# Optimization experiments

Measured on AMD Instinct MI355X. Metric: run time of the kernel, lower is better.

Reference implementation:

```python
import jax, jax.numpy as jnp
import numpy as np

B, D, H, W, C = 4, 8, 16, 16, 512
K_RED = 8
R = C // K_RED          # reduced channels for Q/K
EPS = 1e-3              # keras LayerNormalization default epsilon


def setup_inputs() -> dict:
    key = jax.random.key(0)
    ks = jax.random.split(key, 8)
    s = 0.02
    f32 = jnp.float32
    return {
        "x":  jax.random.normal(ks[0], (B, D, H, W, C), f32),
        # 1x1x1 Conv3D == per-position linear over channels
        "wq": (jax.random.normal(ks[1], (C, R), f32) * s), "bq": jnp.zeros((R,), f32),
        "wk": (jax.random.normal(ks[2], (C, R), f32) * s), "bk": jnp.zeros((R,), f32),
        "wv": (jax.random.normal(ks[3], (C, C), f32) * s), "bv": jnp.zeros((C,), f32),
        "wm": (jax.random.normal(ks[4], (C, C), f32) * s), "bm": jnp.zeros((C,), f32),
        "g1": jnp.ones((C,), f32), "b1": jnp.zeros((C,), f32),
        "g2": jnp.ones((C,), f32), "b2": jnp.zeros((C,), f32),
    }


def _layer_norm(x, g, b):
    m = jnp.mean(x, axis=-1, keepdims=True)
    v = jnp.mean(jnp.square(x - m), axis=-1, keepdims=True)
    return (x - m) * jax.lax.rsqrt(v + EPS) * g + b


def reference(x, wq, bq, wk, bk, wv, bv, wm, bm, g1, b1, g2, b2):
    b, d, h, w, c = x.shape
    f = h * w
    xf = x.reshape(b, d, f, c)                      # [B,D,F,C]
    Q = xf @ wq + bq                                # [B,D,F,R]
    K = xf @ wk + bk                                # [B,D,F,R]
    V = xf @ wv + bv                                # [B,D,F,C]
    # full global scores: [B, D, F, D, F]
    e = jnp.einsum('bifr,bgjr->bifgj', Q, K)
    alphas = jax.nn.softmax(e.reshape(b, d, f, d * f), axis=-1)
    alphas = alphas.reshape(b, d, f, d, f)
    # original einsum 'bdfgh,bdhi->bdfi' sums over key-depth g and uses V at
    # the query depth d; fold the g-sum first, then per-depth F x F matmul.
    a2 = alphas.sum(axis=3)                         # [B,D,F,F]
    attn = jnp.einsum('bdfh,bdhc->bdfc', a2, V)     # [B,D,F,C]
    y1 = _layer_norm(attn + xf, g1, b1)
    y2 = _layer_norm(y1 + jax.nn.relu(y1 @ wm + bm), g2, b2)
    return y2.reshape(b, d, h, w, c)
```

## Files before the change

kernel.cpp:

```cpp
#include <hip/hip_runtime.h>
#include <cstdint>

#define LN_EPS 1e-3f
using u16 = unsigned short;
using u32 = unsigned int;
typedef __attribute__((ext_vector_type(8))) short bh8;
typedef __attribute__((ext_vector_type(4))) float f4;
#define MFMA16(A,B,C) __builtin_amdgcn_mfma_f32_16x16x32_bf16((A),(B),(C),0,0,0)

__device__ __forceinline__ u16 bf16r(float f){
    union{float f;u32 u;} c; c.f=f;
    return (u16)((c.u + 0x7fffu + ((c.u>>16)&1u))>>16);
}
__device__ __forceinline__ u32 pk2(float a, float b){
    return (u32)bf16r(a) | ((u32)bf16r(b)<<16);
}
__device__ __forceinline__ void glds16(const void* g, void* l){
    __builtin_amdgcn_global_load_lds(
        (const __attribute__((address_space(1))) u32*)g,
        (__attribute__((address_space(3))) u32*)l, 16, 0, 0);
}

__global__ __launch_bounds__(256) void k0_prep(
    const float* __restrict__ wq, const float* __restrict__ wk,
    const float* __restrict__ wv, const float* __restrict__ wm,
    u16* __restrict__ wqkv_p, u16* __restrict__ wm_p)
{
    const int t = threadIdx.x;
    const int c = t & 15, qn = t >> 4;
    const int quad = qn & 3, ntl = qn >> 2;
    const int blk = blockIdx.x;
    if (blk < 32){
        const int s = blk >> 1, hh = blk & 1;
        const int krow = s*32 + quad*8;
        u16* dst = wqkv_p + (size_t)s*20480;
        #pragma unroll
        for (int i=0;i<5;++i){
            const int nt = hh*20 + i*4 + ntl;
            const int n = nt*16 + c;
            const float* src; int ldw;
            if (n < 64){ src = wq + (size_t)krow*64 + n; ldw = 64; }
            else if (n < 128){ src = wk + (size_t)krow*64 + (n-64); ldw = 64; }
            else { src = wv + (size_t)krow*512 + (n-128); ldw = 512; }
            float v[8];
            #pragma unroll
            for (int j=0;j<8;++j) v[j] = src[(size_t)j*ldw];
            uint4 o; o.x=pk2(v[0],v[1]); o.y=pk2(v[2],v[3]); o.z=pk2(v[4],v[5]); o.w=pk2(v[6],v[7]);
            *(uint4*)&dst[((nt*4+quad)*16 + c)*8] = o;
        }
    } else {
        const int bb = blk - 32;
        const int s = bb >> 1, hh = bb & 1;
        const int krow = s*32 + quad*8;
        u16* dst = wm_p + (size_t)s*16384;
        #pragma unroll
        for (int i=0;i<4;++i){
            const int nt = hh*16 + i*4 + ntl;
            const int n = nt*16 + c;
            const float* src = wm + (size_t)krow*512 + n;
            float v[8];
            #pragma unroll
            for (int j=0;j<8;++j) v[j] = src[(size_t)j*512];
            uint4 o; o.x=pk2(v[0],v[1]); o.y=pk2(v[2],v[3]); o.z=pk2(v[4],v[5]); o.w=pk2(v[6],v[7]);
            *(uint4*)&dst[((nt*4+quad)*16 + c)*8] = o;
        }
    }
}

__global__ __launch_bounds__(512) void k1_qkv(
    const float* __restrict__ x, const float* __restrict__ bq, const float* __restrict__ bk,
    const u16* __restrict__ wqkv_p,
    u16* __restrict__ Qb, u16* __restrict__ Kb, u16* __restrict__ Vb)
{
    __shared__ u16 Asf[16384];
    __shared__ u16 Bs[2][20480];
    const int t = threadIdx.x, w = t>>6, lane = t&63, quad = (lane>>4)&3, c = lane&15;
    const int rg = w>>2, cg = w&3;
    const int rowbase = blockIdx.x << 5;

    #pragma unroll
    for (int i=0;i<8;++i){
        const int idx = t + (i<<9);
        const int fr = idx >> 7, fc4 = idx & 127;
        float4 xv = *(const float4*)&x[(size_t)(rowbase+fr)*512 + fc4*4];
        uint2 pkv; pkv.x = pk2(xv.x,xv.y); pkv.y = pk2(xv.z,xv.w);
        const int s = fc4 >> 3, qd = (fc4 >> 1) & 3, j0 = (fc4 & 1)*4;
        *(uint2*)&Asf[(fr>>4)*8192 + s*512 + (qd*16 + (fr&15))*8 + j0] = pkv;
    }
    f4 acc[10];
    #pragma unroll
    for (int i=0;i<10;++i) acc[i] = (f4){0.f,0.f,0.f,0.f};
    #pragma unroll
    for (int i=0;i<5;++i)
        glds16((const char*)wqkv_p + (size_t)w*5120 + i*1024 + lane*16,
               (char*)Bs[0] + w*5120 + i*1024);
    __syncthreads();

    for (int s=0;s<16;++s){
        const u16* Bcur = Bs[s&1];
        if (s+1 < 16){
            #pragma unroll
            for (int i=0;i<5;++i)
                glds16((const char*)wqkv_p + (size_t)(s+1)*40960 + (size_t)w*5120 + i*1024 + lane*16,
                       (char*)Bs[(s+1)&1] + w*5120 + i*1024);
        }
        bh8 a = *(const bh8*)&Asf[rg*8192 + s*512 + (quad*16+c)*8];
        #pragma unroll
        for (int nt2=0;nt2<10;++nt2){
            bh8 bb = *(const bh8*)&Bcur[((cg*10+nt2)*4 + quad)*128 + c*8];
            acc[nt2] = MFMA16(a, bb, acc[nt2]);
        }
        __syncthreads();
    }

    const int rt = (blockIdx.x<<1) + rg;
    const int bd = rowbase >> 8;
    const int kloc = (rowbase & 255) + rg*16 + quad*4;
    const int sv = kloc >> 5, kq = (kloc >> 3) & 3, jk0 = kloc & 7;
    #pragma unroll
    for (int nt2=0;nt2<10;++nt2){
        const int colb = cg*160 + nt2*16;
        if (colb < 128){
            const bool isK = (colb >= 64);
            const int r = colb - (isK ? 64 : 0) + c;
            const float bias = isK ? bk[r] : bq[r];
            u16* dstb = (isK ? Kb : Qb) + ((size_t)(rt*2 + (r>>5))*4 + ((r>>3)&3))*128 + (r&7);
            #pragma unroll
            for (int reg=0;reg<4;++reg)
                dstb[(quad*4+reg)*8] = bf16r(acc[nt2][reg] + bias);
        } else {
            const int ntv = (colb - 128) >> 4;
            u16* dstv = Vb + (size_t)bd*131072 + (size_t)sv*16384
                           + (size_t)((ntv*4+kq)*128 + c*8 + jk0);
            ushort4 o;
            o.x = bf16r(acc[nt2][0]); o.y = bf16r(acc[nt2][1]);
            o.z = bf16r(acc[nt2][2]); o.w = bf16r(acc[nt2][3]);
            *(ushort4*)dstv = o;
        }
    }
}

__global__ __launch_bounds__(512) void k234(
    const u16* __restrict__ Qb, const u16* __restrict__ Kb, const u16* __restrict__ Vb,
    const u16* __restrict__ wm_p,
    const float* __restrict__ x, const float* __restrict__ bv,
    const float* __restrict__ g1, const float* __restrict__ b1,
    const float* __restrict__ bm, const float* __restrict__ g2, const float* __restrict__ b2,
    float* __restrict__ out)
{
    __shared__ u16 Bs[2][16384];
    __shared__ u16 y1f[16384];
    __shared__ u16 a2f[8192];
    __shared__ u16 qsf[2048];
    __shared__ float redA[2][4][16], redB[2][4][16];
    const int t = threadIdx.x, w = t>>6, lane = t&63, quad = (lane>>4)&3, c = lane&15;
    const int rg = w>>2, cg = w&3;
    const int bd = blockIdx.x & 31, ftile = blockIdx.x >> 5;
    const int b = bd >> 3;
    const int rowbase = (bd<<8) + (ftile<<5);
    const int rt00 = rowbase >> 4;
    const char* Kbase = (const char*)Kb + (size_t)b*262144;
    const char* Vbase = (const char*)Vb + (size_t)bd*262144;

    if (w < 4) glds16((const char*)Qb + (size_t)rt00*2048 + w*1024 + lane*16,
                      (char*)qsf + w*1024);
    #pragma unroll
    for (int i=0;i<2;++i)
        glds16(Kbase + (size_t)w*2048 + i*1024 + lane*16, (char*)Bs[0] + w*2048 + i*1024);
    __syncthreads();
    bh8 aq0 = *(const bh8*)&qsf[rg*1024 + (quad*16+c)*8];
    bh8 aq1 = *(const bh8*)&qsf[rg*1024 + 512 + (quad*16+c)*8];

    float lp[4] = {0.f,0.f,0.f,0.f};
    float a2r[4][2][2] = {};
    #pragma unroll
    for (int cc=0; cc<16; ++cc){
        const u16* Bcur = Bs[cc&1];
        if (cc+1 < 16){
            #pragma unroll
            for (int i=0;i<2;++i)
                glds16(Kbase + (size_t)(cc+1)*16384 + (size_t)w*2048 + i*1024 + lane*16,
                       (char*)Bs[(cc+1)&1] + w*2048 + i*1024);
        }
        f4 sa[2] = { (f4){0.f,0.f,0.f,0.f}, (f4){0.f,0.f,0.f,0.f} };
        #pragma unroll
        for (int kt=0;kt<2;++kt){
            bh8 b0 = *(const bh8*)&Bcur[(cg*2+kt)*1024 + (quad*16+c)*8];
            bh8 b1v= *(const bh8*)&Bcur[(cg*2+kt)*1024 + 512 + (quad*16+c)*8];
            sa[kt] = MFMA16(aq0, b0, sa[kt]);
            sa[kt] = MFMA16(aq1, b1v, sa[kt]);
        }
        #pragma unroll
        for (int kt=0;kt<2;++kt)
            #pragma unroll
            for (int reg=0;reg<4;++reg){
                float e = __expf(sa[kt][reg]);
                lp[reg] += e;
                a2r[reg][cc&1][kt] += e;
            }
        __syncthreads();
    }
    {
        #pragma unroll
        for (int i=0;i<4;++i)
            glds16(Vbase + (size_t)w*4096 + i*1024 + lane*16, (char*)Bs[0] + w*4096 + i*1024);
    }
    #pragma unroll
    for (int reg=0;reg<4;++reg){
        float v = lp[reg];
        v += __shfl_xor(v,1,64); v += __shfl_xor(v,2,64);
        v += __shfl_xor(v,4,64); v += __shfl_xor(v,8,64);
        lp[reg] = v;
    }
    if (c==0){
        #pragma unroll
        for (int reg=0;reg<4;++reg) redA[rg][cg][quad*4+reg] = lp[reg];
    }
    __syncthreads();
    float fac[4];
    #pragma unroll
    for (int reg=0;reg<4;++reg){
        const int q = quad*4+reg;
        fac[reg] = 1.f/(redA[rg][0][q]+redA[rg][1][q]+redA[rg][2][q]+redA[rg][3][q]);
    }
    #pragma unroll
    for (int reg=0;reg<4;++reg)
        #pragma unroll
        for (int h=0;h<2;++h)
            #pragma unroll
            for (int kt=0;kt<2;++kt){
                const int jp = h*128 + cg*32 + kt*16 + c;
                a2f[rg*4096 + (jp>>5)*512 + (((jp>>3)&3)*16 + quad*4+reg)*8 + (jp&7)]
                    = bf16r(a2r[reg][h][kt]*fac[reg]);
            }
    __syncthreads();

    f4 cacc[8];
    #pragma unroll
    for (int i=0;i<8;++i) cacc[i] = (f4){0.f,0.f,0.f,0.f};
    for (int s8=0;s8<8;++s8){
        const u16* Bcur = Bs[s8&1];
        if (s8+1 < 8){
            #pragma unroll
            for (int i=0;i<4;++i)
                glds16(Vbase + (size_t)(s8+1)*32768 + (size_t)w*4096 + i*1024 + lane*16,
                       (char*)Bs[(s8+1)&1] + w*4096 + i*1024);
        }
        bh8 a = *(const bh8*)&a2f[rg*4096 + s8*512 + (quad*16+c)*8];
        #pragma unroll
        for (int nt2=0;nt2<8;++nt2){
            bh8 bb = *(const bh8*)&Bcur[((cg*8+nt2)*4 + quad)*128 + c*8];
            cacc[nt2] = MFMA16(a, bb, cacc[nt2]);
        }
        __syncthreads();
    }

    {
        float sv4[4] = {0.f,0.f,0.f,0.f}, qv2[4] = {0.f,0.f,0.f,0.f};
        #pragma unroll
        for (int nt2=0;nt2<8;++nt2){
            const int col = cg*128 + nt2*16 + c;
            const float bvv = bv[col];
            #pragma unroll
            for (int reg=0;reg<4;++reg){
                const int row = rowbase + rg*16 + quad*4 + reg;
                float val = cacc[nt2][reg] + bvv + x[(size_t)row*512 + col];
                cacc[nt2][reg] = val;
                sv4[reg] += val; qv2[reg] = fmaf(val,val,qv2[reg]);
            }
        }
        #pragma unroll
        for (int reg=0;reg<4;++reg){
            float s1=sv4[reg], s2=qv2[reg];
            s1 += __shfl_xor(s1,1,64); s2 += __shfl_xor(s2,1,64);
            s1 += __shfl_xor(s1,2,64); s2 += __shfl_xor(s2,2,64);
            s1 += __shfl_xor(s1,4,64); s2 += __shfl_xor(s2,4,64);
            s1 += __shfl_xor(s1,8,64); s2 += __shfl_xor(s2,8,64);
            sv4[reg]=s1; qv2[reg]=s2;
        }
        if (c==0){
            #pragma unroll
            for (int reg=0;reg<4;++reg){ redA[rg][cg][quad*4+reg]=sv4[reg]; redB[rg][cg][quad*4+reg]=qv2[reg]; }
        }
        __syncthreads();
        float mean[4], rstd[4];
        #pragma unroll
        for (int reg=0;reg<4;++reg){
            const int q = quad*4+reg;
            const float S  = redA[rg][0][q]+redA[rg][1][q]+redA[rg][2][q]+redA[rg][3][q];
            const float Q2 = redB[rg][0][q]+redB[rg][1][q]+redB[rg][2][q]+redB[rg][3][q];
            const float m = S*(1.f/512.f);
            mean[reg]=m; rstd[reg]=rsqrtf(Q2*(1.f/512.f) - m*m + LN_EPS);
        }
        #pragma unroll
        for (int nt2=0;nt2<8;++nt2){
            const int col = cg*128 + nt2*16 + c;
            const float gg = g1[col], bb1 = b1[col];
            #pragma unroll
            for (int reg=0;reg<4;++reg){
                float y = (cacc[nt2][reg]-mean[reg])*rstd[reg]*gg + bb1;
                cacc[nt2][reg] = y;
                y1f[rg*8192 + (col>>5)*512 + (((col>>3)&3)*16 + quad*4+reg)*8 + (col&7)] = bf16r(y);
            }
        }
        #pragma unroll
        for (int i=0;i<4;++i)
            glds16((const char*)wm_p + (size_t)w*4096 + i*1024 + lane*16,
                   (char*)Bs[0] + w*4096 + i*1024);
        __syncthreads();
    }

    f4 dacc[8];
    #pragma unroll
    for (int i=0;i<8;++i) dacc[i] = (f4){0.f,0.f,0.f,0.f};
    for (int s=0;s<16;++s){
        const u16* Bcur = Bs[s&1];
        if (s+1 < 16){
            #pragma unroll
            for (int i=0;i<4;++i)
                glds16((const char*)wm_p + (size_t)(s+1)*32768 + (size_t)w*4096 + i*1024 + lane*16,
                       (char*)Bs[(s+1)&1] + w*4096 + i*1024);
        }
        bh8 a = *(const bh8*)&y1f[rg*8192 + s*512 + (quad*16+c)*8];
        #pragma unroll
        for (int nt2=0;nt2<8;++nt2){
            bh8 bb = *(const bh8*)&Bcur[((cg*8+nt2)*4 + quad)*128 + c*8];
            dacc[nt2] = MFMA16(a, bb, dacc[nt2]);
        }
        __syncthreads();
    }

    {
        float sv4[4] = {0.f,0.f,0.f,0.f}, qv2[4] = {0.f,0.f,0.f,0.f};
        #pragma unroll
        for (int nt2=0;nt2<8;++nt2){
            const int col = cg*128 + nt2*16 + c;
            const float bmv = bm[col];
            #pragma unroll
            for (int reg=0;reg<4;++reg){
                float hh = fmaxf(dacc[nt2][reg]+bmv, 0.f) + cacc[nt2][reg];
                dacc[nt2][reg] = hh;
                sv4[reg] += hh; qv2[reg] = fmaf(hh,hh,qv2[reg]);
            }
        }
        #pragma unroll
        for (int reg=0;reg<4;++reg){
            float s1=sv4[reg], s2=qv2[reg];
            s1 += __shfl_xor(s1,1,64); s2 += __shfl_xor(s2,1,64);
            s1 += __shfl_xor(s1,2,64); s2 += __shfl_xor(s2,2,64);
            s1 += __shfl_xor(s1,4,64); s2 += __shfl_xor(s2,4,64);
            s1 += __shfl_xor(s1,8,64); s2 += __shfl_xor(s2,8,64);
            sv4[reg]=s1; qv2[reg]=s2;
        }
        if (c==0){
            #pragma unroll
            for (int reg=0;reg<4;++reg){ redA[rg][cg][quad*4+reg]=sv4[reg]; redB[rg][cg][quad*4+reg]=qv2[reg]; }
        }
        __syncthreads();
        float mean[4], rstd[4];
        #pragma unroll
        for (int reg=0;reg<4;++reg){
            const int q = quad*4+reg;
            const float S  = redA[rg][0][q]+redA[rg][1][q]+redA[rg][2][q]+redA[rg][3][q];
            const float Q2 = redB[rg][0][q]+redB[rg][1][q]+redB[rg][2][q]+redB[rg][3][q];
            const float m = S*(1.f/512.f);
            mean[reg]=m; rstd[reg]=rsqrtf(Q2*(1.f/512.f) - m*m + LN_EPS);
        }
        #pragma unroll
        for (int nt2=0;nt2<8;++nt2){
            const int col = cg*128 + nt2*16 + c;
            const float gg = g2[col], bb2 = b2[col];
            #pragma unroll
            for (int reg=0;reg<4;++reg){
                const int row = rowbase + rg*16 + quad*4 + reg;
                out[(size_t)row*512 + col] = (dacc[nt2][reg]-mean[reg])*rstd[reg]*gg + bb2;
            }
        }
    }
}

extern "C" void kernel_launch(void* const* d_in, const int* in_sizes, int n_in,
                              void* d_out, int out_size, void* d_ws, size_t ws_size,
                              hipStream_t stream) {
    (void)in_sizes; (void)n_in; (void)out_size; (void)ws_size;
    const float* x  = (const float*)d_in[0];
    const float* wq = (const float*)d_in[1];
    const float* bq = (const float*)d_in[2];
    const float* wk = (const float*)d_in[3];
    const float* bk = (const float*)d_in[4];
    const float* wv = (const float*)d_in[5];
    const float* bv = (const float*)d_in[6];
    const float* wm = (const float*)d_in[7];
    const float* bm = (const float*)d_in[8];
    const float* g1 = (const float*)d_in[9];
    const float* b1 = (const float*)d_in[10];
    const float* g2 = (const float*)d_in[11];
    const float* b2 = (const float*)d_in[12];

    u16* wqkv_p = (u16*)d_ws;
    u16* wm_p   = wqkv_p + 327680;
    u16* Qb     = wm_p   + 262144;
    u16* Kb     = Qb     + 524288;
    u16* Vb     = Kb     + 524288;
    float* outp = (float*)d_out;

    k0_prep<<<64, 256, 0, stream>>>(wq, wk, wv, wm, wqkv_p, wm_p);
    k1_qkv <<<256, 512, 0, stream>>>(x, bq, bk, wqkv_p, Qb, Kb, Vb);
    k234   <<<256, 512, 0, stream>>>(Qb, Kb, Vb, wm_p, x, bv, g1, b1, bm, g2, b2, outp);
}
```

Before: 152.6 us.

## Use explicit vmcnt waits and raw barriers to overlap prefetch with MFMA loops

Replaces __syncthreads in the double-buffered GEMM loops with explicit s_waitcnt vmcnt(N) plus s_barrier, so the next tile's global-to-LDS loads stay in flight while the current tile is consumed. It also raises wave priority around the MFMA bursts and issues the weight prefetch in k1 before the x conversion. In the score phase, K tiles are made twice as large so there are half as many barrier steps. The hand-placed waitcnt counts must match the number of outstanding loads exactly, so a miscount would be a correctness hazard.

```diff
diff --git a/kernel.cpp b/kernel.cpp
--- a/kernel.cpp
+++ b/kernel.cpp
@@ -7,6 +7,9 @@
 typedef __attribute__((ext_vector_type(8))) short bh8;
 typedef __attribute__((ext_vector_type(4))) float f4;
 #define MFMA16(A,B,C) __builtin_amdgcn_mfma_f32_16x16x32_bf16((A),(B),(C),0,0,0)
+#define SBAR() __builtin_amdgcn_s_barrier()
+#define CFENCE() asm volatile("" ::: "memory")
+#define WAITV(N) asm volatile("s_waitcnt vmcnt(" #N ")" ::: "memory")
 
 __device__ __forceinline__ u16 bf16r(float f){
     union{float f;u32 u;} c; c.f=f;
@@ -79,6 +82,10 @@
     const int rowbase = blockIdx.x << 5;
 
     #pragma unroll
+    for (int i=0;i<5;++i)
+        glds16((const char*)wqkv_p + (size_t)w*5120 + i*1024 + lane*16,
+               (char*)Bs[0] + w*5120 + i*1024);
+    #pragma unroll
     for (int i=0;i<8;++i){
         const int idx = t + (i<<9);
         const int fr = idx >> 7, fc4 = idx & 127;
@@ -90,27 +97,29 @@
     f4 acc[10];
     #pragma unroll
     for (int i=0;i<10;++i) acc[i] = (f4){0.f,0.f,0.f,0.f};
-    #pragma unroll
-    for (int i=0;i<5;++i)
-        glds16((const char*)wqkv_p + (size_t)w*5120 + i*1024 + lane*16,
-               (char*)Bs[0] + w*5120 + i*1024);
     __syncthreads();
 
     for (int s=0;s<16;++s){
         const u16* Bcur = Bs[s&1];
+        bh8 a = *(const bh8*)&Asf[rg*8192 + s*512 + (quad*16+c)*8];
         if (s+1 < 16){
             #pragma unroll
             for (int i=0;i<5;++i)
                 glds16((const char*)wqkv_p + (size_t)(s+1)*40960 + (size_t)w*5120 + i*1024 + lane*16,
                        (char*)Bs[(s+1)&1] + w*5120 + i*1024);
-        }
-        bh8 a = *(const bh8*)&Asf[rg*8192 + s*512 + (quad*16+c)*8];
+            WAITV(5);
+        } else {
+            WAITV(0);
+        }
+        SBAR(); CFENCE();
+        __builtin_amdgcn_s_setprio(1);
         #pragma unroll
         for (int nt2=0;nt2<10;++nt2){
             bh8 bb = *(const bh8*)&Bcur[((cg*10+nt2)*4 + quad)*128 + c*8];
             acc[nt2] = MFMA16(a, bb, acc[nt2]);
         }
-        __syncthreads();
+        __builtin_amdgcn_s_setprio(0);
+        CFENCE(); SBAR();
     }
 
     const int rt = (blockIdx.x<<1) + rg;
@@ -165,46 +174,50 @@
     if (w < 4) glds16((const char*)Qb + (size_t)rt00*2048 + w*1024 + lane*16,
                       (char*)qsf + w*1024);
     #pragma unroll
-    for (int i=0;i<2;++i)
-        glds16(Kbase + (size_t)w*2048 + i*1024 + lane*16, (char*)Bs[0] + w*2048 + i*1024);
+    for (int i=0;i<4;++i)
+        glds16(Kbase + (size_t)w*4096 + i*1024 + lane*16, (char*)Bs[0] + w*4096 + i*1024);
     __syncthreads();
     bh8 aq0 = *(const bh8*)&qsf[rg*1024 + (quad*16+c)*8];
     bh8 aq1 = *(const bh8*)&qsf[rg*1024 + 512 + (quad*16+c)*8];
 
     float lp[4] = {0.f,0.f,0.f,0.f};
-    float a2r[4][2][2] = {};
-    #pragma unroll
-    for (int cc=0; cc<16; ++cc){
+    float a2r[4][4] = {};
+    for (int cc=0; cc<8; ++cc){
         const u16* Bcur = Bs[cc&1];
-        if (cc+1 < 16){
-            #pragma unroll
-            for (int i=0;i<2;++i)
-                glds16(Kbase + (size_t)(cc+1)*16384 + (size_t)w*2048 + i*1024 + lane*16,
-                       (char*)Bs[(cc+1)&1] + w*2048 + i*1024);
-        }
-        f4 sa[2] = { (f4){0.f,0.f,0.f,0.f}, (f4){0.f,0.f,0.f,0.f} };
-        #pragma unroll
-        for (int kt=0;kt<2;++kt){
-            bh8 b0 = *(const bh8*)&Bcur[(cg*2+kt)*1024 + (quad*16+c)*8];
-            bh8 b1v= *(const bh8*)&Bcur[(cg*2+kt)*1024 + 512 + (quad*16+c)*8];
+        if (cc+1 < 8){
+            #pragma unroll
+            for (int i=0;i<4;++i)
+                glds16(Kbase + (size_t)(cc+1)*32768 + (size_t)w*4096 + i*1024 + lane*16,
+                       (char*)Bs[(cc+1)&1] + w*4096 + i*1024);
+            WAITV(4);
+        } else {
+            WAITV(0);
+        }
+        SBAR(); CFENCE();
+        __builtin_amdgcn_s_setprio(1);
+        f4 sa[4];
+        #pragma unroll
+        for (int kt=0;kt<4;++kt){
+            sa[kt] = (f4){0.f,0.f,0.f,0.f};
+            bh8 b0 = *(const bh8*)&Bcur[(cg*4+kt)*1024 + (quad*16+c)*8];
+            bh8 bv1= *(const bh8*)&Bcur[(cg*4+kt)*1024 + 512 + (quad*16+c)*8];
             sa[kt] = MFMA16(aq0, b0, sa[kt]);
-            sa[kt] = MFMA16(aq1, b1v, sa[kt]);
-        }
-        #pragma unroll
-        for (int kt=0;kt<2;++kt)
+            sa[kt] = MFMA16(aq1, bv1, sa[kt]);
+        }
+        __builtin_amdgcn_s_setprio(0);
+        #pragma unroll
+        for (int kt=0;kt<4;++kt)
             #pragma unroll
             for (int reg=0;reg<4;++reg){
                 float e = __expf(sa[kt][reg]);
                 lp[reg] += e;
-                a2r[reg][cc&1][kt] += e;
+                a2r[reg][kt] += e;
             }
-        __syncthreads();
-    }
-    {
-        #pragma unroll
-        for (int i=0;i<4;++i)
-            glds16(Vbase + (size_t)w*4096 + i*1024 + lane*16, (char*)Bs[0] + w*4096 + i*1024);
-    }
+        CFENCE(); SBAR();
+    }
+    #pragma unroll
+    for (int i=0;i<4;++i)
+        glds16(Vbase + (size_t)w*4096 + i*1024 + lane*16, (char*)Bs[0] + w*4096 + i*1024);
     #pragma unroll
     for (int reg=0;reg<4;++reg){
         float v = lp[reg];
@@ -226,13 +239,11 @@
     #pragma unroll
     for (int reg=0;reg<4;++reg)
         #pragma unroll
-        for (int h=0;h<2;++h)
-            #pragma unroll
-            for (int kt=0;kt<2;++kt){
-                const int jp = h*128 + cg*32 + kt*16 + c;
-                a2f[rg*4096 + (jp>>5)*512 + (((jp>>3)&3)*16 + quad*4+reg)*8 + (jp&7)]
-                    = bf16r(a2r[reg][h][kt]*fac[reg]);
-            }
+        for (int kt=0;kt<4;++kt){
+            const int jp = cg*64 + kt*16 + c;
+            a2f[rg*4096 + (jp>>5)*512 + (((jp>>3)&3)*16 + quad*4+reg)*8 + (jp&7)]
+                = bf16r(a2r[reg][kt]*fac[reg]);
+        }
     __syncthreads();
 
     f4 cacc[8];
@@ -240,19 +251,25 @@
     for (int i=0;i<8;++i) cacc[i] = (f4){0.f,0.f,0.f,0.f};
     for (int s8=0;s8<8;++s8){
         const u16* Bcur = Bs[s8&1];
+        bh8 a = *(const bh8*)&a2f[rg*4096 + s8*512 + (quad*16+c)*8];
         if (s8+1 < 8){
             #pragma unroll
             for (int i=0;i<4;++i)
                 glds16(Vbase + (size_t)(s8+1)*32768 + (size_t)w*4096 + i*1024 + lane*16,
                        (char*)Bs[(s8+1)&1] + w*4096 + i*1024);
-        }
-        bh8 a = *(const bh8*)&a2f[rg*4096 + s8*512 + (quad*16+c)*8];
+            WAITV(4);
+        } else {
+            WAITV(0);
+        }
+        SBAR(); CFENCE();
+        __builtin_amdgcn_s_setprio(1);
         #pragma unroll
         for (int nt2=0;nt2<8;++nt2){
             bh8 bb = *(const bh8*)&Bcur[((cg*8+nt2)*4 + quad)*128 + c*8];
             cacc[nt2] = MFMA16(a, bb, cacc[nt2]);
         }
-        __syncthreads();
+        __builtin_amdgcn_s_setprio(0);
+        CFENCE(); SBAR();
     }
 
     {
@@ -315,19 +332,25 @@
     for (int i=0;i<8;++i) dacc[i] = (f4){0.f,0.f,0.f,0.f};
     for (int s=0;s<16;++s){
         const u16* Bcur = Bs[s&1];
+        bh8 a = *(const bh8*)&y1f[rg*8192 + s*512 + (quad*16+c)*8];
         if (s+1 < 16){
             #pragma unroll
             for (int i=0;i<4;++i)
                 glds16((const char*)wm_p + (size_t)(s+1)*32768 + (size_t)w*4096 + i*1024 + lane*16,
                        (char*)Bs[(s+1)&1] + w*4096 + i*1024);
-        }
-        bh8 a = *(const bh8*)&y1f[rg*8192 + s*512 + (quad*16+c)*8];
+            WAITV(4);
+        } else {
+            WAITV(0);
+        }
+        SBAR(); CFENCE();
+        __builtin_amdgcn_s_setprio(1);
         #pragma unroll
         for (int nt2=0;nt2<8;++nt2){
             bh8 bb = *(const bh8*)&Bcur[((cg*8+nt2)*4 + quad)*128 + c*8];
             dacc[nt2] = MFMA16(a, bb, dacc[nt2]);
         }
-        __syncthreads();
+        __builtin_amdgcn_s_setprio(0);
+        CFENCE(); SBAR();
     }
 
     {
```

Result: faster. 143.9 us (-5.7%).

## Load weight/K/V fragments directly into registers instead of LDS double-buffering

Applied to the files above, without the earlier changes.

Both the QKV projection and the fused attention/MLP kernel stop staging B operands (weights, K, V) through LDS with global_load_lds and per-step barriers. Instead each wave owns a column slice across both row tiles and prefetches its MFMA B fragments straight from global into registers, one step ahead. Most __syncthreads are replaced by a lighter lgkmcnt-wait barrier, and LDS usage shrinks to a single shared buffer, which should allow higher occupancy. In exchange each wave now issues more global loads with less reuse, relying on L2 for the shared operands, and register pressure rises.

```diff
diff --git a/kernel.cpp b/kernel.cpp
--- a/kernel.cpp
+++ b/kernel.cpp
@@ -7,6 +7,8 @@
 typedef __attribute__((ext_vector_type(8))) short bh8;
 typedef __attribute__((ext_vector_type(4))) float f4;
 #define MFMA16(A,B,C) __builtin_amdgcn_mfma_f32_16x16x32_bf16((A),(B),(C),0,0,0)
+#define LKBAR() do{ asm volatile("s_waitcnt lgkmcnt(0)" ::: "memory"); \
+                    __builtin_amdgcn_s_barrier(); asm volatile("" ::: "memory"); }while(0)
 
 __device__ __forceinline__ u16 bf16r(float f){
     union{float f;u32 u;} c; c.f=f;
@@ -14,11 +16,6 @@
 }
 __device__ __forceinline__ u32 pk2(float a, float b){
     return (u32)bf16r(a) | ((u32)bf16r(b)<<16);
-}
-__device__ __forceinline__ void glds16(const void* g, void* l){
-    __builtin_amdgcn_global_load_lds(
-        (const __attribute__((address_space(1))) u32*)g,
-        (__attribute__((address_space(3))) u32*)l, 16, 0, 0);
 }
 
 __global__ __launch_bounds__(256) void k0_prep(
@@ -73,9 +70,7 @@
     u16* __restrict__ Qb, u16* __restrict__ Kb, u16* __restrict__ Vb)
 {
     __shared__ u16 Asf[16384];
-    __shared__ u16 Bs[2][20480];
     const int t = threadIdx.x, w = t>>6, lane = t&63, quad = (lane>>4)&3, c = lane&15;
-    const int rg = w>>2, cg = w&3;
     const int rowbase = blockIdx.x << 5;
 
     #pragma unroll
@@ -87,55 +82,66 @@
         const int s = fc4 >> 3, qd = (fc4 >> 1) & 3, j0 = (fc4 & 1)*4;
         *(uint2*)&Asf[(fr>>4)*8192 + s*512 + (qd*16 + (fr&15))*8 + j0] = pkv;
     }
-    f4 acc[10];
-    #pragma unroll
-    for (int i=0;i<10;++i) acc[i] = (f4){0.f,0.f,0.f,0.f};
-    #pragma unroll
-    for (int i=0;i<5;++i)
-        glds16((const char*)wqkv_p + (size_t)w*5120 + i*1024 + lane*16,
-               (char*)Bs[0] + w*5120 + i*1024);
+    f4 acc[2][5];
+    #pragma unroll
+    for (int rt=0;rt<2;++rt)
+        #pragma unroll
+        for (int i=0;i<5;++i) acc[rt][i] = (f4){0.f,0.f,0.f,0.f};
+    bh8 bw[5];
+    #pragma unroll
+    for (int nt2=0;nt2<5;++nt2)
+        bw[nt2] = *(const bh8*)&wqkv_p[(size_t)((w*5+nt2)*4 + quad)*128 + c*8];
     __syncthreads();
 
+    #pragma unroll
     for (int s=0;s<16;++s){
-        const u16* Bcur = Bs[s&1];
+        bh8 bn[5];
         if (s+1 < 16){
             #pragma unroll
-            for (int i=0;i<5;++i)
-                glds16((const char*)wqkv_p + (size_t)(s+1)*40960 + (size_t)w*5120 + i*1024 + lane*16,
-                       (char*)Bs[(s+1)&1] + w*5120 + i*1024);
-        }
-        bh8 a = *(const bh8*)&Asf[rg*8192 + s*512 + (quad*16+c)*8];
-        #pragma unroll
-        for (int nt2=0;nt2<10;++nt2){
-            bh8 bb = *(const bh8*)&Bcur[((cg*10+nt2)*4 + quad)*128 + c*8];
-            acc[nt2] = MFMA16(a, bb, acc[nt2]);
-        }
-        __syncthreads();
-    }
-
-    const int rt = (blockIdx.x<<1) + rg;
+            for (int nt2=0;nt2<5;++nt2)
+                bn[nt2] = *(const bh8*)&wqkv_p[(size_t)(s+1)*20480 + ((w*5+nt2)*4 + quad)*128 + c*8];
+        }
+        bh8 a[2];
+        #pragma unroll
+        for (int rt=0;rt<2;++rt)
+            a[rt] = *(const bh8*)&Asf[rt*8192 + s*512 + (quad*16+c)*8];
+        #pragma unroll
+        for (int rt=0;rt<2;++rt)
+            #pragma unroll
+            for (int nt2=0;nt2<5;++nt2)
+                acc[rt][nt2] = MFMA16(a[rt], bw[nt2], acc[rt][nt2]);
+        if (s+1 < 16){
+            #pragma unroll
+            for (int nt2=0;nt2<5;++nt2) bw[nt2] = bn[nt2];
+        }
+    }
+
     const int bd = rowbase >> 8;
-    const int kloc = (rowbase & 255) + rg*16 + quad*4;
-    const int sv = kloc >> 5, kq = (kloc >> 3) & 3, jk0 = kloc & 7;
-    #pragma unroll
-    for (int nt2=0;nt2<10;++nt2){
-        const int colb = cg*160 + nt2*16;
-        if (colb < 128){
-            const bool isK = (colb >= 64);
-            const int r = colb - (isK ? 64 : 0) + c;
-            const float bias = isK ? bk[r] : bq[r];
-            u16* dstb = (isK ? Kb : Qb) + ((size_t)(rt*2 + (r>>5))*4 + ((r>>3)&3))*128 + (r&7);
-            #pragma unroll
-            for (int reg=0;reg<4;++reg)
-                dstb[(quad*4+reg)*8] = bf16r(acc[nt2][reg] + bias);
-        } else {
-            const int ntv = (colb - 128) >> 4;
-            u16* dstv = Vb + (size_t)bd*131072 + (size_t)sv*16384
-                           + (size_t)((ntv*4+kq)*128 + c*8 + jk0);
-            ushort4 o;
-            o.x = bf16r(acc[nt2][0]); o.y = bf16r(acc[nt2][1]);
-            o.z = bf16r(acc[nt2][2]); o.w = bf16r(acc[nt2][3]);
-            *(ushort4*)dstv = o;
+    #pragma unroll
+    for (int rt=0;rt<2;++rt){
+        const int rtg = (blockIdx.x<<1) + rt;
+        const int kloc = (rowbase & 255) + rt*16 + quad*4;
+        const int sv = kloc >> 5, kq = (kloc >> 3) & 3, jk0 = kloc & 7;
+        #pragma unroll
+        for (int nt2=0;nt2<5;++nt2){
+            const int colb = w*80 + nt2*16;
+            if (colb < 128){
+                const bool isK = (colb >= 64);
+                const int r = colb - (isK ? 64 : 0) + c;
+                const float bias = isK ? bk[r] : bq[r];
+                u16* dstb = (isK ? Kb : Qb) + ((size_t)(rtg*2 + (r>>5))*4 + ((r>>3)&3))*128 + (r&7);
+                #pragma unroll
+                for (int reg=0;reg<4;++reg)
+                    dstb[(quad*4+reg)*8] = bf16r(acc[rt][nt2][reg] + bias);
+            } else {
+                const int ntv = (colb - 128) >> 4;
+                u16* dstv = Vb + (size_t)bd*131072 + (size_t)sv*16384
+                               + (size_t)((ntv*4+kq)*128 + c*8 + jk0);
+                ushort4 o;
+                o.x = bf16r(acc[rt][nt2][0]); o.y = bf16r(acc[rt][nt2][1]);
+                o.z = bf16r(acc[rt][nt2][2]); o.w = bf16r(acc[rt][nt2][3]);
+                *(ushort4*)dstv = o;
+            }
         }
     }
 }
@@ -148,232 +154,287 @@
     const float* __restrict__ bm, const float* __restrict__ g2, const float* __restrict__ b2,
     float* __restrict__ out)
 {
-    __shared__ u16 Bs[2][16384];
-    __shared__ u16 y1f[16384];
-    __shared__ u16 a2f[8192];
-    __shared__ u16 qsf[2048];
-    __shared__ float redA[2][4][16], redB[2][4][16];
+    __shared__ u16 U[16384];
+    __shared__ float redA[256], redB[256];
     const int t = threadIdx.x, w = t>>6, lane = t&63, quad = (lane>>4)&3, c = lane&15;
-    const int rg = w>>2, cg = w&3;
     const int bd = blockIdx.x & 31, ftile = blockIdx.x >> 5;
     const int b = bd >> 3;
     const int rowbase = (bd<<8) + (ftile<<5);
     const int rt00 = rowbase >> 4;
-    const char* Kbase = (const char*)Kb + (size_t)b*262144;
-    const char* Vbase = (const char*)Vb + (size_t)bd*262144;
-
-    if (w < 4) glds16((const char*)Qb + (size_t)rt00*2048 + w*1024 + lane*16,
-                      (char*)qsf + w*1024);
-    #pragma unroll
-    for (int i=0;i<2;++i)
-        glds16(Kbase + (size_t)w*2048 + i*1024 + lane*16, (char*)Bs[0] + w*2048 + i*1024);
-    __syncthreads();
-    bh8 aq0 = *(const bh8*)&qsf[rg*1024 + (quad*16+c)*8];
-    bh8 aq1 = *(const bh8*)&qsf[rg*1024 + 512 + (quad*16+c)*8];
-
-    float lp[4] = {0.f,0.f,0.f,0.f};
-    float a2r[4][2][2] = {};
-    #pragma unroll
-    for (int cc=0; cc<16; ++cc){
-        const u16* Bcur = Bs[cc&1];
-        if (cc+1 < 16){
-            #pragma unroll
-            for (int i=0;i<2;++i)
-                glds16(Kbase + (size_t)(cc+1)*16384 + (size_t)w*2048 + i*1024 + lane*16,
-                       (char*)Bs[(cc+1)&1] + w*2048 + i*1024);
-        }
-        f4 sa[2] = { (f4){0.f,0.f,0.f,0.f}, (f4){0.f,0.f,0.f,0.f} };
-        #pragma unroll
-        for (int kt=0;kt<2;++kt){
-            bh8 b0 = *(const bh8*)&Bcur[(cg*2+kt)*1024 + (quad*16+c)*8];
-            bh8 b1v= *(const bh8*)&Bcur[(cg*2+kt)*1024 + 512 + (quad*16+c)*8];
-            sa[kt] = MFMA16(aq0, b0, sa[kt]);
-            sa[kt] = MFMA16(aq1, b1v, sa[kt]);
-        }
+    const u16* Kp = Kb + (size_t)b*131072;
+    const u16* Vp = Vb + (size_t)bd*131072;
+
+    bh8 aq[2][2];
+    #pragma unroll
+    for (int rt=0;rt<2;++rt)
+        #pragma unroll
+        for (int kk=0;kk<2;++kk)
+            aq[rt][kk] = *(const bh8*)&Qb[(size_t)(rt00+rt)*1024 + kk*512 + (quad*16+c)*8];
+
+    float lp[2][4] = {};
+    float a2r[2][2][4] = {};
+    bh8 bk0[2][2];
+    #pragma unroll
+    for (int kt=0;kt<2;++kt)
+        #pragma unroll
+        for (int kk=0;kk<2;++kk)
+            bk0[kt][kk] = *(const bh8*)&Kp[(size_t)(w*2+kt)*1024 + kk*512 + (quad*16+c)*8];
+    #pragma unroll
+    for (int cc=0; cc<8; ++cc){
+        bh8 bn[2][2];
+        if (cc+1 < 8){
+            #pragma unroll
+            for (int kt=0;kt<2;++kt)
+                #pragma unroll
+                for (int kk=0;kk<2;++kk)
+                    bn[kt][kk] = *(const bh8*)&Kp[(size_t)((cc+1)*16 + w*2+kt)*1024 + kk*512 + (quad*16+c)*8];
+        }
+        #pragma unroll
+        for (int rt=0;rt<2;++rt)
+            #pragma unroll
+            for (int kt=0;kt<2;++kt){
+                f4 sa = (f4){0.f,0.f,0.f,0.f};
+                sa = MFMA16(aq[rt][0], bk0[kt][0], sa);
+                sa = MFMA16(aq[rt][1], bk0[kt][1], sa);
+                #pragma unroll
+                for (int reg=0;reg<4;++reg){
+                    float e = __expf(sa[reg]);
+                    lp[rt][reg] += e;
+                    a2r[rt][kt][reg] += e;
+                }
+            }
+        if (cc+1 < 8){
+            #pragma unroll
+            for (int kt=0;kt<2;++kt)
+                #pragma unroll
+                for (int kk=0;kk<2;++kk) bk0[kt][kk] = bn[kt][kk];
+        }
+    }
+    bh8 bv8[4];
+    #pragma unroll
+    for (int nt2=0;nt2<4;++nt2)
+        bv8[nt2] = *(const bh8*)&Vp[(size_t)((w*4+nt2)*4 + quad)*128 + c*8];
+    #pragma unroll
+    for (int rt=0;rt<2;++rt)
+        #pragma unroll
+        for (int reg=0;reg<4;++reg){
+            float v = lp[rt][reg];
+            v += __shfl_xor(v,1,64); v += __shfl_xor(v,2,64);
+            v += __shfl_xor(v,4,64); v += __shfl_xor(v,8,64);
+            lp[rt][reg] = v;
+        }
+    if (c==0){
+        #pragma unroll
+        for (int rt=0;rt<2;++rt)
+            #pragma unroll
+            for (int reg=0;reg<4;++reg) redA[w*32 + rt*16 + quad*4+reg] = lp[rt][reg];
+    }
+    LKBAR();
+    float fac[2][4];
+    #pragma unroll
+    for (int rt=0;rt<2;++rt)
+        #pragma unroll
+        for (int reg=0;reg<4;++reg){
+            const int q = rt*16 + quad*4 + reg;
+            float s = 0.f;
+            #pragma unroll
+            for (int ww=0;ww<8;++ww) s += redA[ww*32 + q];
+            fac[rt][reg] = 1.f/s;
+        }
+    #pragma unroll
+    for (int rt=0;rt<2;++rt)
         #pragma unroll
         for (int kt=0;kt<2;++kt)
             #pragma unroll
             for (int reg=0;reg<4;++reg){
-                float e = __expf(sa[kt][reg]);
-                lp[reg] += e;
-                a2r[reg][cc&1][kt] += e;
-            }
-        __syncthreads();
-    }
+                const int jp = w*32 + kt*16 + c;
+                U[rt*4096 + (jp>>5)*512 + (((jp>>3)&3)*16 + quad*4+reg)*8 + (jp&7)]
+                    = bf16r(a2r[rt][kt][reg]*fac[rt][reg]);
+            }
+    LKBAR();
+
+    f4 cacc[2][4];
+    #pragma unroll
+    for (int rt=0;rt<2;++rt)
+        #pragma unroll
+        for (int i=0;i<4;++i) cacc[rt][i] = (f4){0.f,0.f,0.f,0.f};
+    #pragma unroll
+    for (int s8=0;s8<8;++s8){
+        bh8 bn[4];
+        if (s8+1 < 8){
+            #pragma unroll
+            for (int nt2=0;nt2<4;++nt2)
+                bn[nt2] = *(const bh8*)&Vp[(size_t)(s8+1)*16384 + ((w*4+nt2)*4 + quad)*128 + c*8];
+        }
+        bh8 a[2];
+        #pragma unroll
+        for (int rt=0;rt<2;++rt)
+            a[rt] = *(const bh8*)&U[rt*4096 + s8*512 + (quad*16+c)*8];
+        #pragma unroll
+        for (int rt=0;rt<2;++rt)
+            #pragma unroll
+            for (int nt2=0;nt2<4;++nt2)
+                cacc[rt][nt2] = MFMA16(a[rt], bv8[nt2], cacc[rt][nt2]);
+        if (s8+1 < 8){
+            #pragma unroll
+            for (int nt2=0;nt2<4;++nt2) bv8[nt2] = bn[nt2];
+        }
+    }
+    bh8 bm8[4];
+    #pragma unroll
+    for (int nt2=0;nt2<4;++nt2)
+        bm8[nt2] = *(const bh8*)&wm_p[(size_t)((w*4+nt2)*4 + quad)*128 + c*8];
+
+    float mean1[2][4], rstd1[2][4];
     {
-        #pragma unroll
-        for (int i=0;i<4;++i)
-            glds16(Vbase + (size_t)w*4096 + i*1024 + lane*16, (char*)Bs[0] + w*4096 + i*1024);
-    }
-    #pragma unroll
-    for (int reg=0;reg<4;++reg){
-        float v = lp[reg];
-        v += __shfl_xor(v,1,64); v += __shfl_xor(v,2,64);
-        v += __shfl_xor(v,4,64); v += __shfl_xor(v,8,64);
-        lp[reg] = v;
-    }
-    if (c==0){
-        #pragma unroll
-        for (int reg=0;reg<4;++reg) redA[rg][cg][quad*4+reg] = lp[reg];
-    }
-    __syncthreads();
-    float fac[4];
-    #pragma unroll
-    for (int reg=0;reg<4;++reg){
-        const int q = quad*4+reg;
-        fac[reg] = 1.f/(redA[rg][0][q]+redA[rg][1][q]+redA[rg][2][q]+redA[rg][3][q]);
-    }
-    #pragma unroll
-    for (int reg=0;reg<4;++reg)
-        #pragma unroll
-        for (int h=0;h<2;++h)
-            #pragma unroll
-            for (int kt=0;kt<2;++kt){
-                const int jp = h*128 + cg*32 + kt*16 + c;
-                a2f[rg*4096 + (jp>>5)*512 + (((jp>>3)&3)*16 + quad*4+reg)*8 + (jp&7)]
-                    = bf16r(a2r[reg][h][kt]*fac[reg]);
-            }
-    __syncthreads();
-
-    f4 cacc[8];
-    #pragma unroll
-    for (int i=0;i<8;++i) cacc[i] = (f4){0.f,0.f,0.f,0.f};
-    for (int s8=0;s8<8;++s8){
-        const u16* Bcur = Bs[s8&1];
-        if (s8+1 < 8){
-            #pragma unroll
-            for (int i=0;i<4;++i)
-                glds16(Vbase + (size_t)(s8+1)*32768 + (size_t)w*4096 + i*1024 + lane*16,
-                       (char*)Bs[(s8+1)&1] + w*4096 + i*1024);
-        }
-        bh8 a = *(const bh8*)&a2f[rg*4096 + s8*512 + (quad*16+c)*8];
-        #pragma unroll
-        for (int nt2=0;nt2<8;++nt2){
-            bh8 bb = *(const bh8*)&Bcur[((cg*8+nt2)*4 + quad)*128 + c*8];
-            cacc[nt2] = MFMA16(a, bb, cacc[nt2]);
-        }
-        __syncthreads();
+        float sv4[2][4] = {}, qv2[2][4] = {};
+        #pragma unroll
+        for (int rt=0;rt<2;++rt)
+            #pragma unroll
+            for (int nt2=0;nt2<4;++nt2){
+                const int col = w*64 + nt2*16 + c;
+                const float bvv = bv[col];
+                #pragma unroll
+                for (int reg=0;reg<4;++reg){
+                    const int row = rowbase + rt*16 + quad*4 + reg;
+                    float val = cacc[rt][nt2][reg] + bvv + x[(size_t)row*512 + col];
+                    cacc[rt][nt2][reg] = val;
+                    sv4[rt][reg] += val; qv2[rt][reg] = fmaf(val,val,qv2[rt][reg]);
+                }
+            }
+        #pragma unroll
+        for (int rt=0;rt<2;++rt)
+            #pragma unroll
+            for (int reg=0;reg<4;++reg){
+                float s1=sv4[rt][reg], s2=qv2[rt][reg];
+                s1 += __shfl_xor(s1,1,64); s2 += __shfl_xor(s2,1,64);
+                s1 += __shfl_xor(s1,2,64); s2 += __shfl_xor(s2,2,64);
+                s1 += __shfl_xor(s1,4,64); s2 += __shfl_xor(s2,4,64);
+                s1 += __shfl_xor(s1,8,64); s2 += __shfl_xor(s2,8,64);
+                sv4[rt][reg]=s1; qv2[rt][reg]=s2;
+            }
+        if (c==0){
+            #pragma unroll
+            for (int rt=0;rt<2;++rt)
+                #pragma unroll
+                for (int reg=0;reg<4;++reg){
+                    redA[w*32 + rt*16 + quad*4+reg]=sv4[rt][reg];
+                    redB[w*32 + rt*16 + quad*4+reg]=qv2[rt][reg];
+                }
+        }
+        LKBAR();
+        #pragma unroll
+        for (int rt=0;rt<2;++rt)
+            #pragma unroll
+            for (int reg=0;reg<4;++reg){
+                const int q = rt*16 + quad*4 + reg;
+                float S=0.f, Q2=0.f;
+                #pragma unroll
+                for (int ww=0;ww<8;++ww){ S += redA[ww*32+q]; Q2 += redB[ww*32+q]; }
+                const float m = S*(1.f/512.f);
+                mean1[rt][reg]=m; rstd1[rt][reg]=rsqrtf(Q2*(1.f/512.f) - m*m + LN_EPS);
+            }
+        #pragma unroll
+        for (int rt=0;rt<2;++rt)
+            #pragma unroll
+            for (int nt2=0;nt2<4;++nt2){
+                const int col = w*64 + nt2*16 + c;
+                const float gg = g1[col], bb1 = b1[col];
+                #pragma unroll
+                for (int reg=0;reg<4;++reg){
+                    float y = (cacc[rt][nt2][reg]-mean1[rt][reg])*rstd1[rt][reg]*gg + bb1;
+                    cacc[rt][nt2][reg] = y;
+                    U[rt*8192 + (col>>5)*512 + (((col>>3)&3)*16 + quad*4+reg)*8 + (col&7)] = bf16r(y);
+                }
+            }
+        LKBAR();
+    }
+
+    f4 dacc[2][4];
+    #pragma unroll
+    for (int rt=0;rt<2;++rt)
+        #pragma unroll
+        for (int i=0;i<4;++i) dacc[rt][i] = (f4){0.f,0.f,0.f,0.f};
+    #pragma unroll
+    for (int s=0;s<16;++s){
+        bh8 bn[4];
+        if (s+1 < 16){
+            #pragma unroll
+            for (int nt2=0;nt2<4;++nt2)
+                bn[nt2] = *(const bh8*)&wm_p[(size_t)(s+1)*16384 + ((w*4+nt2)*4 + quad)*128 + c*8];
+        }
+        bh8 a[2];
+        #pragma unroll
+        for (int rt=0;rt<2;++rt)
+            a[rt] = *(const bh8*)&U[rt*8192 + s*512 + (quad*16+c)*8];
+        #pragma unroll
+        for (int rt=0;rt<2;++rt)
+            #pragma unroll
+            for (int nt2=0;nt2<4;++nt2)
+                dacc[rt][nt2] = MFMA16(a[rt], bm8[nt2], dacc[rt][nt2]);
+        if (s+1 < 16){
+            #pragma unroll
+            for (int nt2=0;nt2<4;++nt2) bm8[nt2] = bn[nt2];
+        }
     }
 
     {
-        float sv4[4] = {0.f,0.f,0.f,0.f}, qv2[4] = {0.f,0.f,0.f,0.f};
-        #pragma unroll
-        for (int nt2=0;nt2<8;++nt2){
-            const int col = cg*128 + nt2*16 + c;
-            const float bvv = bv[col];
+        float sv4[2][4] = {}, qv2[2][4] = {};
+        #pragma unroll
+        for (int rt=0;rt<2;++rt)
+            #pragma unroll
+            for (int nt2=0;nt2<4;++nt2){
+                const int col = w*64 + nt2*16 + c;
+                const float bmv = bm[col];
+                #pragma unroll
+                for (int reg=0;reg<4;++reg){
+                    float hh = fmaxf(dacc[rt][nt2][reg]+bmv, 0.f) + cacc[rt][nt2][reg];
+                    dacc[rt][nt2][reg] = hh;
+                    sv4[rt][reg] += hh; qv2[rt][reg] = fmaf(hh,hh,qv2[rt][reg]);
+                }
+            }
+        #pragma unroll
+        for (int rt=0;rt<2;++rt)
             #pragma unroll
             for (int reg=0;reg<4;++reg){
-                const int row = rowbase + rg*16 + quad*4 + reg;
-                float val = cacc[nt2][reg] + bvv + x[(size_t)row*512 + col];
-                cacc[nt2][reg] = val;
-                sv4[reg] += val; qv2[reg] = fmaf(val,val,qv2[reg]);
-            }
-        }
-        #pragma unroll
-        for (int reg=0;reg<4;++reg){
-            float s1=sv4[reg], s2=qv2[reg];
-            s1 += __shfl_xor(s1,1,64); s2 += __shfl_xor(s2,1,64);
-            s1 += __shfl_xor(s1,2,64); s2 += __shfl_xor(s2,2,64);
-            s1 += __shfl_xor(s1,4,64); s2 += __shfl_xor(s2,4,64);
-            s1 += __shfl_xor(s1,8,64); s2 += __shfl_xor(s2,8,64);
-            sv4[reg]=s1; qv2[reg]=s2;
-        }
+                float s1=sv4[rt][reg], s2=qv2[rt][reg];
+                s1 += __shfl_xor(s1,1,64); s2 += __shfl_xor(s2,1,64);
+                s1 += __shfl_xor(s1,2,64); s2 += __shfl_xor(s2,2,64);
+                s1 += __shfl_xor(s1,4,64); s2 += __shfl_xor(s2,4,64);
+                s1 += __shfl_xor(s1,8,64); s2 += __shfl_xor(s2,8,64);
+                sv4[rt][reg]=s1; qv2[rt][reg]=s2;
+            }
         if (c==0){
             #pragma unroll
-            for (int reg=0;reg<4;++reg){ redA[rg][cg][quad*4+reg]=sv4[reg]; redB[rg][cg][quad*4+reg]=qv2[reg]; }
-        }
-        __syncthreads();
-        float mean[4], rstd[4];
-        #pragma unroll
-        for (int reg=0;reg<4;++reg){
-            const int q = quad*4+reg;
-            const float S  = redA[rg][0][q]+redA[rg][1][q]+redA[rg][2][q]+redA[rg][3][q];
-            const float Q2 = redB[rg][0][q]+redB[rg][1][q]+redB[rg][2][q]+redB[rg][3][q];
-            const float m = S*(1.f/512.f);
-            mean[reg]=m; rstd[reg]=rsqrtf(Q2*(1.f/512.f) - m*m + LN_EPS);
-        }
-        #pragma unroll
-        for (int nt2=0;nt2<8;++nt2){
-            const int col = cg*128 + nt2*16 + c;
-            const float gg = g1[col], bb1 = b1[col];
+            for (int rt=0;rt<2;++rt)
+                #pragma unroll
+                for (int reg=0;reg<4;++reg){
+                    redA[w*32 + rt*16 + quad*4+reg]=sv4[rt][reg];
+                    redB[w*32 + rt*16 + quad*4+reg]=qv2[rt][reg];
+                }
+        }
+        LKBAR();
+        #pragma unroll
+        for (int rt=0;rt<2;++rt){
+            float mean[4], rstd[4];
             #pragma unroll
             for (int reg=0;reg<4;++reg){
-                float y = (cacc[nt2][reg]-mean[reg])*rstd[reg]*gg + bb1;
-                cacc[nt2][reg] = y;
-                y1f[rg*8192 + (col>>5)*512 + (((col>>3)&3)*16 + quad*4+reg)*8 + (col&7)] = bf16r(y);
-            }
-        }
-        #pragma unroll
-        for (int i=0;i<4;++i)
-            glds16((const char*)wm_p + (size_t)w*4096 + i*1024 + lane*16,
-                   (char*)Bs[0] + w*4096 + i*1024);
-        __syncthreads();
-    }
-
-    f4 dacc[8];
-    #pragma unroll
-    for (int i=0;i<8;++i) dacc[i] = (f4){0.f,0.f,0.f,0.f};
-    for (int s=0;s<16;++s){
-        const u16* Bcur = Bs[s&1];
-        if (s+1 < 16){
-            #pragma unroll
-            for (int i=0;i<4;++i)
-                glds16((const char*)wm_p + (size_t)(s+1)*32768 + (size_t)w*4096 + i*1024 + lane*16,
-                       (char*)Bs[(s+1)&1] + w*4096 + i*1024);
-        }
-        bh8 a = *(const bh8*)&y1f[rg*8192 + s*512 + (quad*16+c)*8];
-        #pragma unroll
-        for (int nt2=0;nt2<8;++nt2){
-            bh8 bb = *(const bh8*)&Bcur[((cg*8+nt2)*4 + quad)*128 + c*8];
-            dacc[nt2] = MFMA16(a, bb, dacc[nt2]);
-        }
-        __syncthreads();
-    }
-
-    {
-        float sv4[4] = {0.f,0.f,0.f,0.f}, qv2[4] = {0.f,0.f,0.f,0.f};
-        #pragma unroll
-        for (int nt2=0;nt2<8;++nt2){
-            const int col = cg*128 + nt2*16 + c;
-            const float bmv = bm[col];
-            #pragma unroll
-            for (int reg=0;reg<4;++reg){
-                float hh = fmaxf(dacc[nt2][reg]+bmv, 0.f) + cacc[nt2][reg];
-                dacc[nt2][reg] = hh;
-                sv4[reg] += hh; qv2[reg] = fmaf(hh,hh,qv2[reg]);
-            }
-        }
-        #pragma unroll
-        for (int reg=0;reg<4;++reg){
-            float s1=sv4[reg], s2=qv2[reg];
-            s1 += __shfl_xor(s1,1,64); s2 += __shfl_xor(s2,1,64);
-            s1 += __shfl_xor(s1,2,64); s2 += __shfl_xor(s2,2,64);
-            s1 += __shfl_xor(s1,4,64); s2 += __shfl_xor(s2,4,64);
-            s1 += __shfl_xor(s1,8,64); s2 += __shfl_xor(s2,8,64);
-            sv4[reg]=s1; qv2[reg]=s2;
-        }
-        if (c==0){
-            #pragma unroll
-            for (int reg=0;reg<4;++reg){ redA[rg][cg][quad*4+reg]=sv4[reg]; redB[rg][cg][quad*4+reg]=qv2[reg]; }
-        }
-        __syncthreads();
-        float mean[4], rstd[4];
-        #pragma unroll
-        for (int reg=0;reg<4;++reg){
-            const int q = quad*4+reg;
-            const float S  = redA[rg][0][q]+redA[rg][1][q]+redA[rg][2][q]+redA[rg][3][q];
-            const float Q2 = redB[rg][0][q]+redB[rg][1][q]+redB[rg][2][q]+redB[rg][3][q];
-            const float m = S*(1.f/512.f);
-            mean[reg]=m; rstd[reg]=rsqrtf(Q2*(1.f/512.f) - m*m + LN_EPS);
-        }
-        #pragma unroll
-        for (int nt2=0;nt2<8;++nt2){
-            const int col = cg*128 + nt2*16 + c;
-            const float gg = g2[col], bb2 = b2[col];
-            #pragma unroll
-            for (int reg=0;reg<4;++reg){
-                const int row = rowbase + rg*16 + quad*4 + reg;
-                out[(size_t)row*512 + col] = (dacc[nt2][reg]-mean[reg])*rstd[reg]*gg + bb2;
+                const int q = rt*16 + quad*4 + reg;
+                float S=0.f, Q2=0.f;
+                #pragma unroll
+                for (int ww=0;ww<8;++ww){ S += redA[ww*32+q]; Q2 += redB[ww*32+q]; }
+                const float m = S*(1.f/512.f);
+                mean[reg]=m; rstd[reg]=rsqrtf(Q2*(1.f/512.f) - m*m + LN_EPS);
+            }
+            #pragma unroll
+            for (int nt2=0;nt2<4;++nt2){
+                const int col = w*64 + nt2*16 + c;
+                const float gg = g2[col], bb2 = b2[col];
+                #pragma unroll
+                for (int reg=0;reg<4;++reg){
+                    const int row = rowbase + rt*16 + quad*4 + reg;
+                    out[(size_t)row*512 + col] = (dacc[rt][nt2][reg]-mean[reg])*rstd[reg]*gg + bb2;
+                }
             }
         }
     }
```

Measured after the change: 127.2 us. 1.2x faster.
